# Kernel optimization log

Hardware: AMD Instinct MI355X
Metric: run time of the kernel (lower is better)

The kernel has to match this reference:

```python
import jax, jax.numpy as jnp
import numpy as np

L = 2       # num_layers
D = 256     # d_model
DFF = 1024  # d_ffn
NH = 8      # n_heads
NP = 4      # n_points
CIN = 512   # in_channels
B = 8
HH = 64
WW = 64
EPS = 1e-5


def setup_inputs() -> dict:
    key = jax.random.key(0)
    ks = iter(jax.random.split(key, 48))
    def w(shape, s=0.02):
        return jax.random.normal(next(ks), shape, jnp.float32) * s
    inp = dict(
        x=jax.random.normal(next(ks), (B, CIN, HH, WW), jnp.float32),
        W_in=w((D, CIN)),
        bn1_g=jnp.ones((D,), jnp.float32), bn1_b=jnp.zeros((D,), jnp.float32),
        bn1_m=jnp.zeros((D,), jnp.float32), bn1_v=jnp.ones((D,), jnp.float32),
        query_embed=w((HH * WW, D), 1.0),
        Woff=w((L, D, NH * NP * 2)), boff=w((L, NH * NP * 2), 2.0),
        Wattn=w((L, D, NH * NP)), battn=jnp.zeros((L, NH * NP), jnp.float32),
        Wval=w((L, D, D)), bval=jnp.zeros((L, D), jnp.float32),
        Wo=w((L, D, D)), bo=jnp.zeros((L, D), jnp.float32),
        ln1_g=jnp.ones((L, D), jnp.float32), ln1_b=jnp.zeros((L, D), jnp.float32),
        W1=w((L, D, DFF)), b1=jnp.zeros((L, DFF), jnp.float32),
        W2=w((L, DFF, D)), b2=jnp.zeros((L, D), jnp.float32),
        ln2_g=jnp.ones((L, D), jnp.float32), ln2_b=jnp.zeros((L, D), jnp.float32),
        W_out=w((CIN, D)),
        bn2_g=jnp.ones((CIN,), jnp.float32), bn2_b=jnp.zeros((CIN,), jnp.float32),
        bn2_m=jnp.zeros((CIN,), jnp.float32), bn2_v=jnp.ones((CIN,), jnp.float32),
    )
    return inp


def layer_norm(x, g, b):
    m = jnp.mean(x, axis=-1, keepdims=True)
    v = jnp.mean((x - m) ** 2, axis=-1, keepdims=True)
    return (x - m) * jax.lax.rsqrt(v + EPS) * g + b


def bilinear_sample(value, loc, Hh, Ww):
    # value: (B, NH, dh, H*W); loc: (B, Lq, NH, NP, 2) normalized to [0,1]
    # Matches F.grid_sample(align_corners=False, padding_mode='zeros') with grid=2*loc-1.
    Bn, Lq, nH, P, _ = loc.shape
    gx = loc[..., 0] * Ww - 0.5
    gy = loc[..., 1] * Hh - 0.5
    x0 = jnp.floor(gx)
    y0 = jnp.floor(gy)
    wx = gx - x0
    wy = gy - y0
    x0i = x0.astype(jnp.int32)
    y0i = y0.astype(jnp.int32)

    def t(a):  # (B,Lq,NH,P) -> (B,NH,1,Lq*P)
        return jnp.transpose(a, (0, 2, 1, 3)).reshape(Bn, nH, 1, Lq * P)

    def gather(xi, yi):
        valid = (xi >= 0) & (xi < Ww) & (yi >= 0) & (yi < Hh)
        xc = jnp.clip(xi, 0, Ww - 1)
        yc = jnp.clip(yi, 0, Hh - 1)
        idx = t(yc * Ww + xc)  # (B,NH,1,Lq*P)
        v = jnp.take_along_axis(value, idx, axis=3)  # (B,NH,dh,Lq*P)
        return v * t(valid).astype(value.dtype)

    v00 = gather(x0i, y0i)
    v10 = gather(x0i + 1, y0i)
    v01 = gather(x0i, y0i + 1)
    v11 = gather(x0i + 1, y0i + 1)
    wxt = t(wx)
    wyt = t(wy)
    out = (v00 * (1 - wxt) * (1 - wyt) + v10 * wxt * (1 - wyt)
           + v01 * (1 - wxt) * wyt + v11 * wxt * wyt)
    return out.reshape(Bn, nH, -1, Lq, P)  # (B,NH,dh,Lq,NP)


def reference(x, W_in, bn1_g, bn1_b, bn1_m, bn1_v, query_embed,
              Woff, boff, Wattn, battn, Wval, bval, Wo, bo,
              ln1_g, ln1_b, W1, b1, W2, b2, ln2_g, ln2_b,
              W_out, bn2_g, bn2_b, bn2_m, bn2_v):
    Bn, C, Hh, Ww = x.shape
    HW = Hh * Ww
    dh = D // NH

    # proj_in: 1x1 conv (no bias) + BN (inference) + ReLU
    xp = jnp.einsum('bchw,dc->bdhw', x, W_in)
    xp = (xp - bn1_m[:, None, None]) * jax.lax.rsqrt(bn1_v[:, None, None] + EPS)
    xp = jax.nn.relu(xp * bn1_g[:, None, None] + bn1_b[:, None, None])
    src = xp.reshape(Bn, D, HW).transpose(0, 2, 1)  # (B, HW, D)

    # reference points: centers of pixels, normalized
    ry = (jnp.arange(Hh, dtype=jnp.float32) + 0.5) / Hh
    rx = (jnp.arange(Ww, dtype=jnp.float32) + 0.5) / Ww
    yy, xx = jnp.meshgrid(ry, rx, indexing='ij')
    refpts = jnp.stack([xx, yy], axis=-1).reshape(HW, 2)  # (HW, 2) as (x, y)
    norm = jnp.array([Ww, Hh], jnp.float32)

    q = jnp.broadcast_to(query_embed[None], (Bn, HW, D))
    for i in range(L):
        # --- MSDeformAttn (n_levels=1) ---
        val = (src @ Wval[i] + bval[i]).reshape(Bn, HW, NH, dh)
        val = val.transpose(0, 2, 3, 1)  # (B, NH, dh, HW)
        off = (q @ Woff[i] + boff[i]).reshape(Bn, HW, NH, NP, 2)
        attn = jax.nn.softmax((q @ Wattn[i] + battn[i]).reshape(Bn, HW, NH, NP), axis=-1)
        loc = refpts[None, :, None, None, :] + off / norm  # (B, HW, NH, NP, 2)
        samp = bilinear_sample(val, loc, Hh, Ww)  # (B, NH, dh, HW, NP)
        o = jnp.einsum('bhdqp,bhqp->bqhd', samp, attn.transpose(0, 2, 1, 3))
        o = o.reshape(Bn, HW, D) @ Wo[i] + bo[i]
        q = layer_norm(q + o, ln1_g[i], ln1_b[i])
        # --- FFN ---
        ffn = jax.nn.relu(q @ W1[i] + b1[i]) @ W2[i] + b2[i]
        q = layer_norm(q + ffn, ln2_g[i], ln2_b[i])

    # proj_out: 1x1 conv (no bias) + BN (inference) + ReLU
    y = q.transpose(0, 2, 1).reshape(Bn, D, Hh, Ww)
    y = jnp.einsum('bdhw,cd->bchw', y, W_out)
    y = (y - bn2_m[:, None, None]) * jax.lax.rsqrt(bn2_v[:, None, None] + EPS)
    return jax.nn.relu(y * bn2_g[:, None, None] + bn2_b[:, None, None])
```

## Files before the change

### kernel.cpp

```cpp
#include <hip/hip_runtime.h>
#include <cstdint>

#define LYR 2
#define DM  256
#define DFFN 1024
#define CINC 512
#define BBATCH 8
#define HWTOT 4096
#define EPSV 1e-5f

using u16 = unsigned short;
typedef __attribute__((ext_vector_type(8))) short bf16x8;
typedef __attribute__((ext_vector_type(4))) float f32x4;

__device__ inline u16 f2b(float v) {
    union { float f; uint32_t u; } x; x.f = v;
    uint32_t r = x.u + 0x7fffu + ((x.u >> 16) & 1u);
    return (u16)(r >> 16);
}
__device__ inline uint32_t pk2(float a, float b) {
    return (uint32_t)f2b(a) | ((uint32_t)f2b(b) << 16);
}
__device__ inline float blo(uint32_t d) {
    union { uint32_t i; float f; } x; x.i = d << 16; return x.f;
}
__device__ inline float bhi(uint32_t d) {
    union { uint32_t i; float f; } x; x.i = d & 0xffff0000u; return x.f;
}

template<int MODE>
__global__ __launch_bounds__(256) void mfma_gemm(
    const u16* __restrict__ A, const u16* __restrict__ Bt,
    const float* __restrict__ scale, const float* __restrict__ shift,
    void* __restrict__ Cv, int M, int N, int K, int ldc,
    long long a_zs, long long b_zs, long long c_zs, int swz, int gxlog)
{
    __shared__ u16 As[4][4096];
    __shared__ u16 Bs[4][4096];
    const int tid = threadIdx.x;
    const int lane = tid & 63;
    const int wid = tid >> 6;
    const int wm = (wid & 1) << 6, wn = (wid >> 1) << 6;
    const int quad = lane >> 4, r = lane & 15;

    int bx = blockIdx.x, by = blockIdx.y;
    if (swz) {
        int linear = by * gridDim.x + bx;
        int xcd = linear & 7;
        int s = linear >> 3;
        bx = s & (gridDim.x - 1);
        by = xcd * (gridDim.y >> 3) + (s >> gxlog);
    }
    const int m0 = by << 7, n0 = bx << 7;
    const u16* Ab = A + (long long)blockIdx.z * a_zs + (long long)m0 * K;
    const u16* Bb = Bt + (long long)blockIdx.z * b_zs + (long long)n0 * K;

    const int u0 = tid, u1 = tid + 256;
    const int mu0 = u0 >> 2, cu0 = (u0 & 3) ^ ((mu0 >> 1) & 3);
    const int mu1 = u1 >> 2, cu1 = (u1 & 3) ^ ((mu1 >> 1) & 3);
    const long long ga0 = (long long)mu0 * K + cu0 * 8;
    const long long ga1 = (long long)mu1 * K + cu1 * 8;

    int aoff[4], boff[4];
#pragma unroll
    for (int t = 0; t < 4; ++t) {
        int m = wm + t * 16 + r;
        aoff[t] = (m * 4 + (quad ^ ((m >> 1) & 3))) * 8;
        int n = wn + t * 16 + r;
        boff[t] = (n * 4 + (quad ^ ((n >> 1) & 3))) * 8;
    }

    f32x4 acc[4][4];
#pragma unroll
    for (int i = 0; i < 4; ++i)
#pragma unroll
        for (int j = 0; j < 4; ++j) acc[i][j] = (f32x4){0.f, 0.f, 0.f, 0.f};

    const int NT = K >> 5;

#define GSTAGE(g, b) do {                                                                       \
    const long long kk = (long long)(g) << 5;                                                   \
    __builtin_amdgcn_global_load_lds((const __attribute__((address_space(1))) void*)(Ab + ga0 + kk), \
        (__attribute__((address_space(3))) void*)(&As[b][u0 * 8]), 16, 0, 0);                   \
    __builtin_amdgcn_global_load_lds((const __attribute__((address_space(1))) void*)(Ab + ga1 + kk), \
        (__attribute__((address_space(3))) void*)(&As[b][u1 * 8]), 16, 0, 0);                   \
    __builtin_amdgcn_global_load_lds((const __attribute__((address_space(1))) void*)(Bb + ga0 + kk), \
        (__attribute__((address_space(3))) void*)(&Bs[b][u0 * 8]), 16, 0, 0);                   \
    __builtin_amdgcn_global_load_lds((const __attribute__((address_space(1))) void*)(Bb + ga1 + kk), \
        (__attribute__((address_space(3))) void*)(&Bs[b][u1 * 8]), 16, 0, 0);                   \
} while (0)

    GSTAGE(0, 0);
    GSTAGE(1, 1);
    GSTAGE(2, 2);

    for (int t = 0; t < NT; ++t) {
        if (t < NT - 2)       asm volatile("s_waitcnt vmcnt(8)" ::: "memory");
        else if (t == NT - 2) asm volatile("s_waitcnt vmcnt(4)" ::: "memory");
        else                  asm volatile("s_waitcnt vmcnt(0)" ::: "memory");
        __builtin_amdgcn_s_barrier();
        __builtin_amdgcn_sched_barrier(0);
        if (t + 3 < NT) GSTAGE(t + 3, (t + 3) & 3);
        const u16* Ap = As[t & 3];
        const u16* Bp = Bs[t & 3];
        bf16x8 af[4], bf[4];
#pragma unroll
        for (int tt = 0; tt < 4; ++tt) af[tt] = *(const bf16x8*)(Ap + aoff[tt]);
#pragma unroll
        for (int tt = 0; tt < 4; ++tt) bf[tt] = *(const bf16x8*)(Bp + boff[tt]);
#pragma unroll
        for (int i = 0; i < 4; ++i)
#pragma unroll
            for (int j = 0; j < 4; ++j)
                acc[i][j] = __builtin_amdgcn_mfma_f32_16x16x32_bf16(bf[j], af[i], acc[i][j], 0, 0, 0);
    }
#undef GSTAGE

    const long long zc = (long long)blockIdx.z * c_zs;
    float4 sh4[4], sc4[4];
    if (MODE != 3) {
#pragma unroll
        for (int j = 0; j < 4; ++j) {
            int colb = n0 + wn + j * 16 + quad * 4;
            sh4[j] = *(const float4*)&shift[colb];
            if (MODE == 1) sc4[j] = *(const float4*)&scale[colb];
        }
    }
#pragma unroll
    for (int i = 0; i < 4; ++i) {
        const int row = m0 + wm + i * 16 + r;
        float rsc = 0.f, rsh = 0.f;
        if (MODE == 3) { rsc = scale[row]; rsh = shift[row]; }
#pragma unroll
        for (int j = 0; j < 4; ++j) {
            const int colb = n0 + wn + j * 16 + quad * 4;
            f32x4 v = acc[i][j];
            if (MODE == 0) {
                uint2 o;
                o.x = pk2(v[0] + sh4[j].x, v[1] + sh4[j].y);
                o.y = pk2(v[2] + sh4[j].z, v[3] + sh4[j].w);
                *(uint2*)((u16*)Cv + zc + (long long)row * ldc + colb) = o;
            } else if (MODE == 1) {
                uint2 o;
                o.x = pk2(fmaxf(v[0] * sc4[j].x + sh4[j].x, 0.f), fmaxf(v[1] * sc4[j].y + sh4[j].y, 0.f));
                o.y = pk2(fmaxf(v[2] * sc4[j].z + sh4[j].z, 0.f), fmaxf(v[3] * sc4[j].w + sh4[j].w, 0.f));
                *(uint2*)((u16*)Cv + zc + (long long)row * ldc + colb) = o;
            } else if (MODE == 2) {
                float4 o = {v[0] + sh4[j].x, v[1] + sh4[j].y, v[2] + sh4[j].z, v[3] + sh4[j].w};
                *(float4*)((float*)Cv + zc + (long long)row * ldc + colb) = o;
            } else {
                float4 o = {fmaxf(v[0] * rsc + rsh, 0.f), fmaxf(v[1] * rsc + rsh, 0.f),
                            fmaxf(v[2] * rsc + rsh, 0.f), fmaxf(v[3] * rsc + rsh, 0.f)};
                *(float4*)((float*)Cv + zc + (long long)row * ldc + colb) = o;
            }
        }
    }
}

__global__ __launch_bounds__(512, 4) void fused_layer(
    const u16* __restrict__ oms, const u16* __restrict__ woF,
    const u16* __restrict__ w1F, const u16* __restrict__ w2F,
    const float* __restrict__ bo, const float* __restrict__ b1, const float* __restrict__ b2,
    float* __restrict__ q, u16* __restrict__ q16,
    const float* __restrict__ g1, const float* __restrict__ be1,
    const float* __restrict__ g2, const float* __restrict__ be2)
{
    __shared__ u16 AqO[16384];
    __shared__ u16 AqQ[16384];
    __shared__ float red_s[8][64], red_ss[8][64];
    const int tid = threadIdx.x;
    const int lane = tid & 63;
    const int w = tid >> 6;
    const int quad = lane >> 4, r = lane & 15;
    const int m0 = blockIdx.x << 6;

    const u16* Ab = oms + (long long)m0 * DM;
#pragma unroll
    for (int i = 0; i < 4; ++i) {
        int u = tid + i * 512;
        int ks = u >> 8, v = u & 255;
        int m = v >> 2, c = (v & 3) ^ ((m >> 1) & 3);
        __builtin_amdgcn_global_load_lds((const __attribute__((address_space(1))) void*)(Ab + (long long)m * DM + ks * 32 + c * 8),
                                         (__attribute__((address_space(3))) void*)(AqO + u * 8), 16, 0, 0);
    }

    int aoff[4];
#pragma unroll
    for (int t = 0; t < 4; ++t) {
        int m = t * 16 + r;
        aoff[t] = (m * 4 + (quad ^ ((m >> 1) & 3))) * 8;
    }

    f32x4 acc[4][2];
#pragma unroll
    for (int i = 0; i < 4; ++i)
#pragma unroll
        for (int j = 0; j < 2; ++j) acc[i][j] = (f32x4){0.f, 0.f, 0.f, 0.f};

    __syncthreads();

#pragma unroll
    for (int ks = 0; ks < 8; ++ks) {
        const u16* bp = woF + ((size_t)(ks * 16 + 2 * w) * 64 + lane) * 8;
        bf16x8 bf0 = *(const bf16x8*)bp;
        bf16x8 bf1 = *(const bf16x8*)(bp + 512);
        bf16x8 af[4];
#pragma unroll
        for (int t = 0; t < 4; ++t) af[t] = *(const bf16x8*)(AqO + ks * 2048 + aoff[t]);
#pragma unroll
        for (int i = 0; i < 4; ++i) {
            acc[i][0] = __builtin_amdgcn_mfma_f32_16x16x32_bf16(bf0, af[i], acc[i][0], 0, 0, 0);
            acc[i][1] = __builtin_amdgcn_mfma_f32_16x16x32_bf16(bf1, af[i], acc[i][1], 0, 0, 0);
        }
    }

    float4 sh2[2];
#pragma unroll
    for (int j = 0; j < 2; ++j)
        sh2[j] = *(const float4*)&bo[w * 32 + j * 16 + quad * 4];

    float s_[4] = {0.f, 0.f, 0.f, 0.f}, ss_[4] = {0.f, 0.f, 0.f, 0.f};
#pragma unroll
    for (int i = 0; i < 4; ++i) {
        const int row = m0 + i * 16 + r;
#pragma unroll
        for (int j = 0; j < 2; ++j) {
            const int colb = w * 32 + j * 16 + quad * 4;
            float4 qo = *(const float4*)&q[(size_t)row * DM + colb];
            acc[i][j][0] += sh2[j].x + qo.x;
            acc[i][j][1] += sh2[j].y + qo.y;
            acc[i][j][2] += sh2[j].z + qo.z;
            acc[i][j][3] += sh2[j].w + qo.w;
#pragma unroll
            for (int e = 0; e < 4; ++e) {
                s_[i] += acc[i][j][e];
                ss_[i] += acc[i][j][e] * acc[i][j][e];
            }
        }
    }
#pragma unroll
    for (int i = 0; i < 4; ++i) {
        s_[i] += __shfl_xor(s_[i], 16);  ss_[i] += __shfl_xor(ss_[i], 16);
        s_[i] += __shfl_xor(s_[i], 32);  ss_[i] += __shfl_xor(ss_[i], 32);
    }
    if (quad == 0) {
#pragma unroll
        for (int i = 0; i < 4; ++i) {
            red_s[w][i * 16 + r] = s_[i];
            red_ss[w][i * 16 + r] = ss_[i];
        }
    }
    __syncthreads();

    float mean[4], rstd[4];
#pragma unroll
    for (int i = 0; i < 4; ++i) {
        float S = 0.f, SS = 0.f;
#pragma unroll
        for (int w2 = 0; w2 < 8; ++w2) { S += red_s[w2][i * 16 + r]; SS += red_ss[w2][i * 16 + r]; }
        mean[i] = S * (1.0f / 256.0f);
        rstd[i] = rsqrtf(SS * (1.0f / 256.0f) - mean[i] * mean[i] + EPSV);
    }

    f32x4 oreg[4][2];
    {
        float4 g4[2], bt4[2];
#pragma unroll
        for (int j = 0; j < 2; ++j) {
            int colb = w * 32 + j * 16 + quad * 4;
            g4[j] = *(const float4*)&g1[colb];
            bt4[j] = *(const float4*)&be1[colb];
        }
#pragma unroll
        for (int i = 0; i < 4; ++i) {
            const int mm = i * 16 + r;
#pragma unroll
            for (int j = 0; j < 2; ++j) {
                float o0 = (acc[i][j][0] - mean[i]) * rstd[i] * g4[j].x + bt4[j].x;
                float o1 = (acc[i][j][1] - mean[i]) * rstd[i] * g4[j].y + bt4[j].y;
                float o2 = (acc[i][j][2] - mean[i]) * rstd[i] * g4[j].z + bt4[j].z;
                float o3 = (acc[i][j][3] - mean[i]) * rstd[i] * g4[j].w + bt4[j].w;
                oreg[i][j] = (f32x4){o0, o1, o2, o3};
                const int pp = (j * 2 + (quad >> 1)) ^ ((r >> 1) & 3);
                *(uint2*)(AqQ + w * 2048 + (mm * 4 + pp) * 8 + (quad & 1) * 4) =
                    make_uint2(pk2(o0, o1), pk2(o2, o3));
            }
        }
    }
    __syncthreads();

    f32x4 acc2[4][2];
#pragma unroll
    for (int i = 0; i < 4; ++i)
#pragma unroll
        for (int j = 0; j < 2; ++j) acc2[i][j] = (f32x4){0.f, 0.f, 0.f, 0.f};

    for (int qq = 0; qq < 4; ++qq) {
        if (qq) __syncthreads();
#pragma unroll
        for (int j = 0; j < 2; ++j) {
            f32x4 a1[4];
#pragma unroll
            for (int i = 0; i < 4; ++i) a1[i] = (f32x4){0.f, 0.f, 0.f, 0.f};
            __builtin_amdgcn_s_setprio(1);
#pragma unroll
            for (int ks = 0; ks < 8; ++ks) {
                const u16* bp = w1F + ((size_t)(ks * 64 + qq * 16 + w * 2 + j) * 64 + lane) * 8;
                bf16x8 bf = *(const bf16x8*)bp;
                bf16x8 af[4];
#pragma unroll
                for (int t = 0; t < 4; ++t) af[t] = *(const bf16x8*)(AqQ + ks * 2048 + aoff[t]);
#pragma unroll
                for (int i = 0; i < 4; ++i)
                    a1[i] = __builtin_amdgcn_mfma_f32_16x16x32_bf16(bf, af[i], a1[i], 0, 0, 0);
            }
            __builtin_amdgcn_s_setprio(0);
            const int cb = qq * 256 + w * 32 + j * 16 + quad * 4;
            const float4 b14 = *(const float4*)&b1[cb];
            const int lane2 = r | (((j * 2 + (quad >> 1)) & 3) << 4);
            const int eo = (quad & 1) * 4;
#pragma unroll
            for (int i = 0; i < 4; ++i) {
                f32x4 v = a1[i];
                uint2 o;
                o.x = pk2(fmaxf(v[0] + b14.x, 0.f), fmaxf(v[1] + b14.y, 0.f));
                o.y = pk2(fmaxf(v[2] + b14.z, 0.f), fmaxf(v[3] + b14.w, 0.f));
                *(uint2*)(AqO + ((w * 4 + i) * 64 + lane2) * 8 + eo) = o;
            }
        }
        __syncthreads();

        __builtin_amdgcn_s_setprio(1);
#pragma unroll
        for (int ks = 0; ks < 8; ++ks) {
            const u16* bp = w2F + ((size_t)((qq * 8 + ks) * 16 + w * 2) * 64 + lane) * 8;
            bf16x8 bf0 = *(const bf16x8*)bp;
            bf16x8 bf1 = *(const bf16x8*)(bp + 512);
            bf16x8 af[4];
#pragma unroll
            for (int t = 0; t < 4; ++t) af[t] = *(const bf16x8*)(AqO + ((ks * 4 + t) * 64 + lane) * 8);
#pragma unroll
            for (int i = 0; i < 4; ++i) {
                acc2[i][0] = __builtin_amdgcn_mfma_f32_16x16x32_bf16(bf0, af[i], acc2[i][0], 0, 0, 0);
                acc2[i][1] = __builtin_amdgcn_mfma_f32_16x16x32_bf16(bf1, af[i], acc2[i][1], 0, 0, 0);
            }
        }
        __builtin_amdgcn_s_setprio(0);
    }

#pragma unroll
    for (int j = 0; j < 2; ++j)
        sh2[j] = *(const float4*)&b2[w * 32 + j * 16 + quad * 4];

#pragma unroll
    for (int i = 0; i < 4; ++i) { s_[i] = 0.f; ss_[i] = 0.f; }
#pragma unroll
    for (int i = 0; i < 4; ++i) {
#pragma unroll
        for (int j = 0; j < 2; ++j) {
            acc2[i][j][0] += sh2[j].x + oreg[i][j][0];
            acc2[i][j][1] += sh2[j].y + oreg[i][j][1];
            acc2[i][j][2] += sh2[j].z + oreg[i][j][2];
            acc2[i][j][3] += sh2[j].w + oreg[i][j][3];
#pragma unroll
            for (int e = 0; e < 4; ++e) {
                s_[i] += acc2[i][j][e];
                ss_[i] += acc2[i][j][e] * acc2[i][j][e];
            }
        }
    }
#pragma unroll
    for (int i = 0; i < 4; ++i) {
        s_[i] += __shfl_xor(s_[i], 16);  ss_[i] += __shfl_xor(ss_[i], 16);
        s_[i] += __shfl_xor(s_[i], 32);  ss_[i] += __shfl_xor(ss_[i], 32);
    }
    if (quad == 0) {
#pragma unroll
        for (int i = 0; i < 4; ++i) {
            red_s[w][i * 16 + r] = s_[i];
            red_ss[w][i * 16 + r] = ss_[i];
        }
    }
    __syncthreads();

#pragma unroll
    for (int i = 0; i < 4; ++i) {
        float S = 0.f, SS = 0.f;
#pragma unroll
        for (int w2 = 0; w2 < 8; ++w2) { S += red_s[w2][i * 16 + r]; SS += red_ss[w2][i * 16 + r]; }
        mean[i] = S * (1.0f / 256.0f);
        rstd[i] = rsqrtf(SS * (1.0f / 256.0f) - mean[i] * mean[i] + EPSV);
    }

    float4 g4[2], bt4[2];
#pragma unroll
    for (int j = 0; j < 2; ++j) {
        int colb = w * 32 + j * 16 + quad * 4;
        g4[j] = *(const float4*)&g2[colb];
        bt4[j] = *(const float4*)&be2[colb];
    }
#pragma unroll
    for (int i = 0; i < 4; ++i) {
        const int row = m0 + i * 16 + r;
#pragma unroll
        for (int j = 0; j < 2; ++j) {
            const int colb = w * 32 + j * 16 + quad * 4;
            float o0 = (acc2[i][j][0] - mean[i]) * rstd[i] * g4[j].x + bt4[j].x;
            float o1 = (acc2[i][j][1] - mean[i]) * rstd[i] * g4[j].y + bt4[j].y;
            float o2 = (acc2[i][j][2] - mean[i]) * rstd[i] * g4[j].z + bt4[j].z;
            float o3 = (acc2[i][j][3] - mean[i]) * rstd[i] * g4[j].w + bt4[j].w;
            *(float4*)&q[(size_t)row * DM + colb] = make_float4(o0, o1, o2, o3);
            *(uint2*)(q16 + (size_t)row * DM + colb) = make_uint2(pk2(o0, o1), pk2(o2, o3));
        }
    }
}

__device__ __attribute__((noinline)) void tconv(const float* src, u16* dst, int K, int N, int tk, int tn)
{
    __shared__ float t[32][33];
    const int tx = threadIdx.x & 31, ty = threadIdx.x >> 5;
#pragma unroll
    for (int i = 0; i < 4; ++i)
        t[ty + i * 8][tx] = src[(size_t)(tk * 32 + ty + i * 8) * N + tn * 32 + tx];
    __syncthreads();
#pragma unroll
    for (int i = 0; i < 4; ++i)
        dst[(size_t)(tn * 32 + ty + i * 8) * K + tk * 32 + tx] = f2b(t[tx][ty + i * 8]);
}

__device__ __attribute__((noinline)) void tconv_oa(const float* Woff, const float* Wattn, u16* dst, int tk, int tn)
{
    __shared__ float t[32][33];
    const int tx = threadIdx.x & 31, ty = threadIdx.x >> 5;
#pragma unroll
    for (int i = 0; i < 4; ++i) {
        int k = tk * 32 + ty + i * 8, n = tn * 32 + tx;
        float v = (n < 64) ? Woff[k * 64 + n] : ((n < 96) ? Wattn[k * 32 + n - 64] : 0.f);
        t[ty + i * 8][tx] = v;
    }
    __syncthreads();
#pragma unroll
    for (int i = 0; i < 4; ++i)
        dst[(size_t)(tn * 32 + ty + i * 8) * 256 + tk * 32 + tx] = f2b(t[tx][ty + i * 8]);
}

__device__ __attribute__((noinline)) void frag_prep(const float* W, u16* dst, int ks, int nc, int N)
{
    __shared__ float t[32][256];
    const int tid = threadIdx.x;
#pragma unroll
    for (int kk = 0; kk < 32; ++kk)
        t[kk][tid] = W[(size_t)(ks * 32 + kk) * N + nc * 256 + tid];
    __syncthreads();
    const int NT16 = N >> 4;
#pragma unroll
    for (int i = 0; i < 4; ++i) {
        int idx = tid + i * 256;
        int nt = idx >> 6, l = idx & 63;
        int n = nt * 16 + (l & 15);
        int kb = (l >> 4) * 8;
        u16 o[8];
#pragma unroll
        for (int e = 0; e < 8; ++e) o[e] = f2b(t[kb + e][n]);
        *(uint4*)(dst + ((size_t)(ks * NT16 + nc * 16 + nt) * 64 + l) * 8) = *(const uint4*)o;
    }
}

__global__ __launch_bounds__(256) void prep_weights(
    const float* __restrict__ Wval, const float* __restrict__ Wo,
    const float* __restrict__ W1, const float* __restrict__ W2,
    const float* __restrict__ Woff, const float* __restrict__ Wattn,
    const float* __restrict__ boff, const float* __restrict__ battn,
    const float* __restrict__ W_in, const float* __restrict__ W_out,
    const float* __restrict__ bn1g, const float* __restrict__ bn1b,
    const float* __restrict__ bn1m, const float* __restrict__ bn1v,
    const float* __restrict__ bn2g, const float* __restrict__ bn2b,
    const float* __restrict__ bn2m, const float* __restrict__ bn2v,
    u16* __restrict__ wvalT, u16* __restrict__ woF, u16* __restrict__ w1F,
    u16* __restrict__ w2F, u16* __restrict__ woaT,
    u16* __restrict__ winC, u16* __restrict__ woutC,
    float* __restrict__ bn1sc, float* __restrict__ bn1sh,
    float* __restrict__ bn2sc, float* __restrict__ bn2sh, float* __restrict__ boa)
{
    int bid = blockIdx.x;
    if (bid < 128) {
        int l = bid >> 6, r2 = bid & 63;
        tconv(Wval + l * 65536, wvalT + l * 65536, 256, 256, r2 & 7, r2 >> 3);
    } else if (bid < 192) {
        int i2 = bid - 128, l = i2 >> 5, r2 = i2 & 31;
        tconv_oa(Woff + l * 16384, Wattn + l * 8192, woaT + l * 32768, r2 & 7, r2 >> 3);
    } else if (bid < 208) {
        int i2 = bid - 192;
        frag_prep(Wo + (i2 >> 3) * 65536, woF + (i2 >> 3) * 65536, i2 & 7, 0, 256);
    } else if (bid < 272) {
        int i2 = bid - 208, l = i2 >> 5, r2 = i2 & 31;
        frag_prep(W1 + l * 262144, w1F + l * 262144, r2 >> 2, r2 & 3, 1024);
    } else if (bid < 336) {
        int i2 = bid - 272;
        frag_prep(W2 + (i2 >> 5) * 262144, w2F + (i2 >> 5) * 262144, i2 & 31, 0, 256);
    } else if (bid < 368) {
        int g2 = bid - 336, base = g2 * 4096, t = threadIdx.x;
#pragma unroll
        for (int k = 0; k < 16; ++k) winC[base + k * 256 + t] = f2b(W_in[base + k * 256 + t]);
    } else if (bid < 400) {
        int g2 = bid - 368, base = g2 * 4096, t = threadIdx.x;
#pragma unroll
        for (int k = 0; k < 16; ++k) woutC[base + k * 256 + t] = f2b(W_out[base + k * 256 + t]);
    } else {
        int t = threadIdx.x;
        { float s = bn1g[t] * rsqrtf(bn1v[t] + EPSV); bn1sc[t] = s; bn1sh[t] = bn1b[t] - bn1m[t] * s; }
        for (int c = 0; c < 2; ++c) {
            int i = c * 256 + t;
            float s = bn2g[i] * rsqrtf(bn2v[i] + EPSV);
            bn2sc[i] = s; bn2sh[i] = bn2b[i] - bn2m[i] * s;
        }
        if (t < 128)
            for (int l = 0; l < 2; ++l)
                boa[l * 128 + t] = (t < 64) ? boff[l * 64 + t]
                                 : ((t < 96) ? battn[l * 32 + t - 64] : 0.f);
    }
}

__global__ __launch_bounds__(256) void transpose_x(const float* __restrict__ x, u16* __restrict__ xT)
{
    __shared__ float t[64][65];
    const int b = blockIdx.z, p0 = blockIdx.y << 6, c0 = blockIdx.x << 6;
    const int tx = threadIdx.x & 63, ty = threadIdx.x >> 6;
    const float* xb = x + ((size_t)b * CINC + c0) * HWTOT + p0;
#pragma unroll
    for (int i = 0; i < 16; ++i)
        t[ty + i * 4][tx] = xb[(size_t)(ty + i * 4) * HWTOT + tx];
    __syncthreads();
    u16* xo = xT + ((size_t)b * HWTOT + p0) * CINC + c0;
#pragma unroll
    for (int i = 0; i < 16; ++i)
        xo[(size_t)(ty + i * 4) * CINC + tx] = f2b(t[tx][ty + i * 4]);
}

struct IW { int eo; float w; };

__global__ __launch_bounds__(256) void sample_kernel(
    const u16* __restrict__ val,
    const float* __restrict__ oa,
    u16* __restrict__ oms)
{
    __shared__ float s_oa[8][96];
    __shared__ IW s_iw[8][32][5];
    const int t = threadIdx.x;
    const int bq0 = blockIdx.x << 3;
    const int b = blockIdx.x >> 9;

    {
        int qi = t >> 5, j = t & 31;
        if (j < 24)
            ((float4*)s_oa[qi])[j] = ((const float4*)oa)[((size_t)(bq0 + qi)) * 32 + j];
    }
    __syncthreads();

    {
        const int qi = t >> 5, hp = t & 31, h = hp >> 2, p = hp & 3;
        const float* so = s_oa[qi];
        float l0 = so[64 + h * 4 + 0], l1 = so[64 + h * 4 + 1];
        float l2 = so[64 + h * 4 + 2], l3 = so[64 + h * 4 + 3];
        float mx = fmaxf(fmaxf(l0, l1), fmaxf(l2, l3));
        float e0 = __expf(l0 - mx), e1 = __expf(l1 - mx), e2 = __expf(l2 - mx), e3 = __expf(l3 - mx);
        float inv = 1.0f / (e0 + e1 + e2 + e3);
        float aw = ((p == 0) ? e0 : (p == 1) ? e1 : (p == 2) ? e2 : e3) * inv;
        const int bq = bq0 + qi;
        float gx = (float)(bq & 63) + so[hp * 2 + 0];
        float gy = (float)((bq >> 6) & 63) + so[hp * 2 + 1];
        float x0f = floorf(gx), y0f = floorf(gy);
        float wx = gx - x0f, wy = gy - y0f;
        int x0 = (int)x0f, y0 = (int)y0f;
#pragma unroll
        for (int c = 0; c < 4; ++c) {
            int xi = x0 + (c & 1), yi = y0 + (c >> 1);
            bool ok = (xi >= 0) && (xi < 64) && (yi >= 0) && (yi < 64);
            float wgt = ((c & 1) ? wx : 1.0f - wx) * ((c >> 1) ? wy : 1.0f - wy);
            s_iw[qi][hp][c].eo = ok ? ((yi * 64 + xi) << 8) : 0;
            s_iw[qi][hp][c].w = ok ? aw * wgt : 0.f;
        }
    }
    __syncthreads();

    {
        const int qi = t >> 5, l = t & 31, h = l >> 2, cc = l & 3;
        const u16* base = val + ((size_t)b << 20) + (h << 5) + (cc << 3);
        float a[8] = {0.f, 0.f, 0.f, 0.f, 0.f, 0.f, 0.f, 0.f};
#pragma unroll
        for (int p = 0; p < 4; ++p)
#pragma unroll
            for (int c = 0; c < 4; ++c) {
                IW iw = s_iw[qi][(h << 2) + p][c];
                uint4 v = *(const uint4*)(base + iw.eo);
                a[0] += iw.w * blo(v.x); a[1] += iw.w * bhi(v.x);
                a[2] += iw.w * blo(v.y); a[3] += iw.w * bhi(v.y);
                a[4] += iw.w * blo(v.z); a[5] += iw.w * bhi(v.z);
                a[6] += iw.w * blo(v.w); a[7] += iw.w * bhi(v.w);
            }
        uint4 o;
        o.x = (uint32_t)f2b(a[0]) | ((uint32_t)f2b(a[1]) << 16);
        o.y = (uint32_t)f2b(a[2]) | ((uint32_t)f2b(a[3]) << 16);
        o.z = (uint32_t)f2b(a[4]) | ((uint32_t)f2b(a[5]) << 16);
        o.w = (uint32_t)f2b(a[6]) | ((uint32_t)f2b(a[7]) << 16);
        *(uint4*)(oms + (size_t)(bq0 + qi) * 256 + (h << 5) + (cc << 3)) = o;
    }
}

__global__ __launch_bounds__(256) void bcast_q(
    const float4* __restrict__ qe, float4* __restrict__ q, u16* __restrict__ q16)
{
    const int i = blockIdx.x * 256 + threadIdx.x;
    float4 v = qe[i];
    uint2 pk = make_uint2(pk2(v.x, v.y), pk2(v.z, v.w));
#pragma unroll
    for (int b = 0; b < BBATCH; ++b) {
        q[(size_t)b * 262144 + i] = v;
        ((uint2*)q16)[(size_t)b * 262144 + i] = pk;
    }
}

extern "C" void kernel_launch(void* const* d_in, const int* in_sizes, int n_in,
                              void* d_out, int out_size, void* d_ws, size_t ws_size,
                              hipStream_t stream)
{
    (void)in_sizes; (void)n_in; (void)out_size; (void)ws_size;
    const float* x     = (const float*)d_in[0];
    const float* W_in  = (const float*)d_in[1];
    const float* bn1_g = (const float*)d_in[2];
    const float* bn1_b = (const float*)d_in[3];
    const float* bn1_m = (const float*)d_in[4];
    const float* bn1_v = (const float*)d_in[5];
    const float* qe    = (const float*)d_in[6];
    const float* Woff  = (const float*)d_in[7];
    const float* boff  = (const float*)d_in[8];
    const float* Wattn = (const float*)d_in[9];
    const float* battn = (const float*)d_in[10];
    const float* Wval  = (const float*)d_in[11];
    const float* bval  = (const float*)d_in[12];
    const float* Wo    = (const float*)d_in[13];
    const float* bo    = (const float*)d_in[14];
    const float* ln1_g = (const float*)d_in[15];
    const float* ln1_b = (const float*)d_in[16];
    const float* W1    = (const float*)d_in[17];
    const float* b1    = (const float*)d_in[18];
    const float* W2    = (const float*)d_in[19];
    const float* b2    = (const float*)d_in[20];
    const float* ln2_g = (const float*)d_in[21];
    const float* ln2_b = (const float*)d_in[22];
    const float* W_out = (const float*)d_in[23];
    const float* bn2_g = (const float*)d_in[24];
    const float* bn2_b = (const float*)d_in[25];
    const float* bn2_m = (const float*)d_in[26];
    const float* bn2_v = (const float*)d_in[27];
    float* out = (float*)d_out;

    char* w = (char*)d_ws;
    char* pool    = w;          w += 67108864;
    float* q      = (float*)w;  w += 33554432;
    u16*  q16     = (u16*)w;    w += 16777216;
    u16*  src16   = (u16*)w;    w += 16777216;
    u16*  wvalT   = (u16*)w;    w += 262144;
    u16*  woF     = (u16*)w;    w += 262144;
    u16*  w1F     = (u16*)w;    w += 1048576;
    u16*  w2F     = (u16*)w;    w += 1048576;
    u16*  woaT    = (u16*)w;    w += 131072;
    u16*  winC    = (u16*)w;    w += 262144;
    u16*  woutC   = (u16*)w;    w += 262144;
    float* bn1sc  = (float*)w;  w += 1024;
    float* bn1sh  = (float*)w;  w += 1024;
    float* bn2sc  = (float*)w;  w += 2048;
    float* bn2sh  = (float*)w;  w += 2048;
    float* boa    = (float*)w;  w += 1024;

    u16*  xT     = (u16*)pool;
    u16*  val16  = (u16*)pool;
    float* offat = (float*)(pool + 16777216);
    u16*  oms16  = (u16*)(pool + 33554432);

    prep_weights<<<dim3(401), 256, 0, stream>>>(
        Wval, Wo, W1, W2, Woff, Wattn, boff, battn, W_in, W_out,
        bn1_g, bn1_b, bn1_m, bn1_v, bn2_g, bn2_b, bn2_m, bn2_v,
        wvalT, woF, w1F, w2F, woaT, winC, woutC, bn1sc, bn1sh, bn2sc, bn2sh, boa);
    transpose_x<<<dim3(CINC / 64, HWTOT / 64, BBATCH), 256, 0, stream>>>(x, xT);
    bcast_q<<<dim3(1024), 256, 0, stream>>>((const float4*)qe, (float4*)q, q16);

    mfma_gemm<1><<<dim3(2, 256, 1), 256, 0, stream>>>(
        xT, winC, bn1sc, bn1sh, src16, 32768, 256, 512, 256, 0, 0, 0, 1, 1);

    for (int l = 0; l < LYR; ++l) {
        mfma_gemm<0><<<dim3(2, 256, 1), 256, 0, stream>>>(
            src16, wvalT + l * 65536, nullptr, bval + l * 256, val16,
            32768, 256, 256, 256, 0, 0, 0, 1, 1);
        mfma_gemm<2><<<dim3(1, 256, 1), 256, 0, stream>>>(
            q16, woaT + l * 32768, nullptr, boa + l * 128, offat,
            32768, 128, 256, 128, 0, 0, 0, 1, 0);
        sample_kernel<<<dim3(4096), 256, 0, stream>>>(val16, offat, oms16);
        fused_layer<<<dim3(512), 512, 0, stream>>>(
            oms16, woF + l * 65536, w1F + l * 262144, w2F + l * 262144,
            bo + l * 256, b1 + l * 1024, b2 + l * 256, q, q16,
            ln1_g + l * 256, ln1_b + l * 256, ln2_g + l * 256, ln2_b + l * 256);
    }

    mfma_gemm<3><<<dim3(32, 4, BBATCH), 256, 0, stream>>>(
        woutC, q16, bn2sc, bn2sh, out, 512, 4096, 256, 4096,
        0, (long long)HWTOT * DM, (long long)CINC * HWTOT, 0, 0);
}
```

Before: 461.3 us.

## Restructure layer loop: batch value projections, fuse next-layer offset GEMM into fused layer

```diff
diff --git a/kernel.cpp b/kernel.cpp
--- a/kernel.cpp
+++ b/kernel.cpp
@@ -157,11 +157,14 @@
     }
 }
 
+template<int WRITEQ, int OA>
 __global__ __launch_bounds__(512, 4) void fused_layer(
     const u16* __restrict__ oms, const u16* __restrict__ woF,
     const u16* __restrict__ w1F, const u16* __restrict__ w2F,
+    const u16* __restrict__ woaF,
     const float* __restrict__ bo, const float* __restrict__ b1, const float* __restrict__ b2,
-    float* __restrict__ q, u16* __restrict__ q16,
+    const float* __restrict__ boa1,
+    float* __restrict__ q, u16* __restrict__ q16, float* __restrict__ offat,
     const float* __restrict__ g1, const float* __restrict__ be1,
     const float* __restrict__ g2, const float* __restrict__ be2)
 {
@@ -409,8 +412,46 @@
             float o1 = (acc2[i][j][1] - mean[i]) * rstd[i] * g4[j].y + bt4[j].y;
             float o2 = (acc2[i][j][2] - mean[i]) * rstd[i] * g4[j].z + bt4[j].z;
             float o3 = (acc2[i][j][3] - mean[i]) * rstd[i] * g4[j].w + bt4[j].w;
-            *(float4*)&q[(size_t)row * DM + colb] = make_float4(o0, o1, o2, o3);
+            oreg[i][j] = (f32x4){o0, o1, o2, o3};
+            if (WRITEQ)
+                *(float4*)&q[(size_t)row * DM + colb] = make_float4(o0, o1, o2, o3);
             *(uint2*)(q16 + (size_t)row * DM + colb) = make_uint2(pk2(o0, o1), pk2(o2, o3));
+        }
+    }
+
+    if (OA) {
+#pragma unroll
+        for (int i = 0; i < 4; ++i) {
+            const int mm = i * 16 + r;
+#pragma unroll
+            for (int j = 0; j < 2; ++j) {
+                const int pp = (j * 2 + (quad >> 1)) ^ ((r >> 1) & 3);
+                *(uint2*)(AqQ + w * 2048 + (mm * 4 + pp) * 8 + (quad & 1) * 4) =
+                    make_uint2(pk2(oreg[i][j][0], oreg[i][j][1]),
+                               pk2(oreg[i][j][2], oreg[i][j][3]));
+            }
+        }
+        __syncthreads();
+        f32x4 aoa[4];
+#pragma unroll
+        for (int i = 0; i < 4; ++i) aoa[i] = (f32x4){0.f, 0.f, 0.f, 0.f};
+#pragma unroll
+        for (int ks = 0; ks < 8; ++ks) {
+            const u16* bp = woaF + ((size_t)(ks * 8 + w) * 64 + lane) * 8;
+            bf16x8 bf = *(const bf16x8*)bp;
+            bf16x8 af[4];
+#pragma unroll
+            for (int t = 0; t < 4; ++t) af[t] = *(const bf16x8*)(AqQ + ks * 2048 + aoff[t]);
+#pragma unroll
+            for (int i = 0; i < 4; ++i)
+                aoa[i] = __builtin_amdgcn_mfma_f32_16x16x32_bf16(bf, af[i], aoa[i], 0, 0, 0);
+        }
+        const float4 bo4 = *(const float4*)&boa1[w * 16 + quad * 4];
+#pragma unroll
+        for (int i = 0; i < 4; ++i) {
+            const int row = m0 + i * 16 + r;
+            float4 o = {aoa[i][0] + bo4.x, aoa[i][1] + bo4.y, aoa[i][2] + bo4.z, aoa[i][3] + bo4.w};
+            *(float4*)&offat[(size_t)row * 128 + w * 16 + quad * 4] = o;
         }
     }
 }
@@ -463,6 +504,32 @@
 #pragma unroll
         for (int e = 0; e < 8; ++e) o[e] = f2b(t[kb + e][n]);
         *(uint4*)(dst + ((size_t)(ks * NT16 + nc * 16 + nt) * 64 + l) * 8) = *(const uint4*)o;
+    }
+}
+
+__device__ __attribute__((noinline)) void frag_prep_oa(const float* Woff, const float* Wattn, u16* dst, int ks)
+{
+    __shared__ float t[32][128];
+    const int tid = threadIdx.x;
+#pragma unroll
+    for (int kk2 = 0; kk2 < 16; ++kk2) {
+        int idx = tid + kk2 * 256;
+        int row = idx >> 7, col = idx & 127;
+        float v = (col < 64) ? Woff[(size_t)(ks * 32 + row) * 64 + col]
+                 : ((col < 96) ? Wattn[(size_t)(ks * 32 + row) * 32 + col - 64] : 0.f);
+        t[row][col] = v;
+    }
+    __syncthreads();
+#pragma unroll
+    for (int u2 = 0; u2 < 2; ++u2) {
+        int unit = tid + u2 * 256;
+        int nt = unit >> 6, l = unit & 63;
+        int n = nt * 16 + (l & 15);
+        int kb = (l >> 4) * 8;
+        u16 o[8];
+#pragma unroll
+        for (int e = 0; e < 8; ++e) o[e] = f2b(t[kb + e][n]);
+        *(uint4*)(dst + ((size_t)(ks * 8 + nt) * 64 + l) * 8) = *(const uint4*)o;
     }
 }
 
@@ -477,7 +544,7 @@
     const float* __restrict__ bn2g, const float* __restrict__ bn2b,
     const float* __restrict__ bn2m, const float* __restrict__ bn2v,
     u16* __restrict__ wvalT, u16* __restrict__ woF, u16* __restrict__ w1F,
-    u16* __restrict__ w2F, u16* __restrict__ woaT,
+    u16* __restrict__ w2F, u16* __restrict__ woaT, u16* __restrict__ woaF,
     u16* __restrict__ winC, u16* __restrict__ woutC,
     float* __restrict__ bn1sc, float* __restrict__ bn1sh,
     float* __restrict__ bn2sc, float* __restrict__ bn2sh, float* __restrict__ boa)
@@ -486,24 +553,26 @@
     if (bid < 128) {
         int l = bid >> 6, r2 = bid & 63;
         tconv(Wval + l * 65536, wvalT + l * 65536, 256, 256, r2 & 7, r2 >> 3);
-    } else if (bid < 192) {
-        int i2 = bid - 128, l = i2 >> 5, r2 = i2 & 31;
-        tconv_oa(Woff + l * 16384, Wattn + l * 8192, woaT + l * 32768, r2 & 7, r2 >> 3);
-    } else if (bid < 208) {
-        int i2 = bid - 192;
+    } else if (bid < 160) {
+        int r2 = bid - 128;
+        tconv_oa(Woff, Wattn, woaT, r2 & 7, r2 >> 3);
+    } else if (bid < 176) {
+        int i2 = bid - 160;
         frag_prep(Wo + (i2 >> 3) * 65536, woF + (i2 >> 3) * 65536, i2 & 7, 0, 256);
-    } else if (bid < 272) {
-        int i2 = bid - 208, l = i2 >> 5, r2 = i2 & 31;
+    } else if (bid < 240) {
+        int i2 = bid - 176, l = i2 >> 5, r2 = i2 & 31;
         frag_prep(W1 + l * 262144, w1F + l * 262144, r2 >> 2, r2 & 3, 1024);
-    } else if (bid < 336) {
-        int i2 = bid - 272;
+    } else if (bid < 304) {
+        int i2 = bid - 240;
         frag_prep(W2 + (i2 >> 5) * 262144, w2F + (i2 >> 5) * 262144, i2 & 31, 0, 256);
-    } else if (bid < 368) {
-        int g2 = bid - 336, base = g2 * 4096, t = threadIdx.x;
+    } else if (bid < 312) {
+        frag_prep_oa(Woff + 16384, Wattn + 8192, woaF, bid - 304);
+    } else if (bid < 344) {
+        int g2 = bid - 312, base = g2 * 4096, t = threadIdx.x;
 #pragma unroll
         for (int k = 0; k < 16; ++k) winC[base + k * 256 + t] = f2b(W_in[base + k * 256 + t]);
-    } else if (bid < 400) {
-        int g2 = bid - 368, base = g2 * 4096, t = threadIdx.x;
+    } else if (bid < 376) {
+        int g2 = bid - 344, base = g2 * 4096, t = threadIdx.x;
 #pragma unroll
         for (int k = 0; k < 16; ++k) woutC[base + k * 256 + t] = f2b(W_out[base + k * 256 + t]);
     } else {
@@ -542,7 +611,8 @@
 __global__ __launch_bounds__(256) void sample_kernel(
     const u16* __restrict__ val,
     const float* __restrict__ oa,
-    u16* __restrict__ oms)
+    u16* __restrict__ oms,
+    int lofs, unsigned int mask)
 {
     __shared__ float s_oa[8][96];
     __shared__ IW s_iw[8][32][5];
@@ -553,7 +623,7 @@
     {
         int qi = t >> 5, j = t & 31;
         if (j < 24)
-            ((float4*)s_oa[qi])[j] = ((const float4*)oa)[((size_t)(bq0 + qi)) * 32 + j];
+            ((float4*)s_oa[qi])[j] = ((const float4*)oa)[((size_t)((bq0 + qi) & mask)) * 32 + j];
     }
     __syncthreads();
 
@@ -577,7 +647,7 @@
             int xi = x0 + (c & 1), yi = y0 + (c >> 1);
             bool ok = (xi >= 0) && (xi < 64) && (yi >= 0) && (yi < 64);
             float wgt = ((c & 1) ? wx : 1.0f - wx) * ((c >> 1) ? wy : 1.0f - wy);
-            s_iw[qi][hp][c].eo = ok ? ((yi * 64 + xi) << 8) : 0;
+            s_iw[qi][hp][c].eo = ok ? ((yi * 64 + xi) << 9) : 0;
             s_iw[qi][hp][c].w = ok ? aw * wgt : 0.f;
         }
     }
@@ -585,7 +655,7 @@
 
     {
         const int qi = t >> 5, l = t & 31, h = l >> 2, cc = l & 3;
-        const u16* base = val + ((size_t)b << 20) + (h << 5) + (cc << 3);
+        const u16* base = val + ((size_t)b << 21) + lofs + (h << 5) + (cc << 3);
         float a[8] = {0.f, 0.f, 0.f, 0.f, 0.f, 0.f, 0.f, 0.f};
 #pragma unroll
         for (int p = 0; p < 4; ++p)
@@ -614,10 +684,9 @@
     float4 v = qe[i];
     uint2 pk = make_uint2(pk2(v.x, v.y), pk2(v.z, v.w));
 #pragma unroll
-    for (int b = 0; b < BBATCH; ++b) {
+    for (int b = 0; b < BBATCH; ++b)
         q[(size_t)b * 262144 + i] = v;
-        ((uint2*)q16)[(size_t)b * 262144 + i] = pk;
-    }
+    ((uint2*)q16)[i] = pk;
 }
 
 extern "C" void kernel_launch(void* const* d_in, const int* in_sizes, int n_in,
@@ -664,7 +733,8 @@
     u16*  woF     = (u16*)w;    w += 262144;
     u16*  w1F     = (u16*)w;    w += 1048576;
     u16*  w2F     = (u16*)w;    w += 1048576;
-    u16*  woaT    = (u16*)w;    w += 131072;
+    u16*  woaT    = (u16*)w;    w += 65536;
+    u16*  woaF    = (u16*)w;    w += 65536;
     u16*  winC    = (u16*)w;    w += 262144;
     u16*  woutC   = (u16*)w;    w += 262144;
     float* bn1sc  = (float*)w;  w += 1024;
@@ -675,32 +745,35 @@
 
     u16*  xT     = (u16*)pool;
     u16*  val16  = (u16*)pool;
-    float* offat = (float*)(pool + 16777216);
-    u16*  oms16  = (u16*)(pool + 33554432);
-
-    prep_weights<<<dim3(401), 256, 0, stream>>>(
+    float* offat = (float*)(pool + 33554432);
+    u16*  oms16  = (u16*)(pool + 50331648);
+
+    prep_weights<<<dim3(377), 256, 0, stream>>>(
         Wval, Wo, W1, W2, Woff, Wattn, boff, battn, W_in, W_out,
         bn1_g, bn1_b, bn1_m, bn1_v, bn2_g, bn2_b, bn2_m, bn2_v,
-        wvalT, woF, w1F, w2F, woaT, winC, woutC, bn1sc, bn1sh, bn2sc, bn2sh, boa);
+        wvalT, woF, w1F, w2F, woaT, woaF, winC, woutC, bn1sc, bn1sh, bn2sc, bn2sh, boa);
     transpose_x<<<dim3(CINC / 64, HWTOT / 64, BBATCH), 256, 0, stream>>>(x, xT);
     bcast_q<<<dim3(1024), 256, 0, stream>>>((const float4*)qe, (float4*)q, q16);
 
     mfma_gemm<1><<<dim3(2, 256, 1), 256, 0, stream>>>(
         xT, winC, bn1sc, bn1sh, src16, 32768, 256, 512, 256, 0, 0, 0, 1, 1);
 
-    for (int l = 0; l < LYR; ++l) {
-        mfma_gemm<0><<<dim3(2, 256, 1), 256, 0, stream>>>(
-            src16, wvalT + l * 65536, nullptr, bval + l * 256, val16,
-            32768, 256, 256, 256, 0, 0, 0, 1, 1);
-        mfma_gemm<2><<<dim3(1, 256, 1), 256, 0, stream>>>(
-            q16, woaT + l * 32768, nullptr, boa + l * 128, offat,
-            32768, 128, 256, 128, 0, 0, 0, 1, 0);
-        sample_kernel<<<dim3(4096), 256, 0, stream>>>(val16, offat, oms16);
-        fused_layer<<<dim3(512), 512, 0, stream>>>(
-            oms16, woF + l * 65536, w1F + l * 262144, w2F + l * 262144,
-            bo + l * 256, b1 + l * 1024, b2 + l * 256, q, q16,
-            ln1_g + l * 256, ln1_b + l * 256, ln2_g + l * 256, ln2_b + l * 256);
-    }
+    mfma_gemm<2><<<dim3(1, 32, 1), 256, 0, stream>>>(
+        q16, woaT, nullptr, boa, offat, 4096, 128, 256, 128, 0, 0, 0, 1, 0);
+
+    mfma_gemm<0><<<dim3(4, 256, 1), 256, 0, stream>>>(
+        src16, wvalT, nullptr, bval, val16, 32768, 512, 256, 512, 0, 0, 0, 1, 2);
+
+    sample_kernel<<<dim3(4096), 256, 0, stream>>>(val16, offat, oms16, 0, 4095u);
+    fused_layer<1, 1><<<dim3(512), 512, 0, stream>>>(
+        oms16, woF, w1F, w2F, woaF, bo, b1, b2, boa + 128, q, q16, offat,
+        ln1_g, ln1_b, ln2_g, ln2_b);
+
+    sample_kernel<<<dim3(4096), 256, 0, stream>>>(val16, offat, oms16, 256, 0xFFFFFFFFu);
+    fused_layer<0, 0><<<dim3(512), 512, 0, stream>>>(
+        oms16, woF + 65536, w1F + 262144, w2F + 262144, nullptr,
+        bo + 256, b1 + 1024, b2 + 256, nullptr, q, q16, nullptr,
+        ln1_g + 256, ln1_b + 256, ln2_g + 256, ln2_b + 256);
 
     mfma_gemm<3><<<dim3(32, 4, BBATCH), 256, 0, stream>>>(
         woutC, q16, bn2sc, bn2sh, out, 512, 4096, 256, 4096,
```

New measurement: 451.2 us. -2.2%, faster.
